# Kernel optimization log

Measured on AMD Instinct MI355X. Metric: run time of the kernel, lower is better.

## Reference

```python
import jax, jax.numpy as jnp
import numpy as np

NEG = -9e15  # matches torch's -9000000000000000.0 masking constant


def setup_inputs() -> dict:
    key = jax.random.key(0)
    kq, kk, kv, ka = jax.random.split(key, 4)
    B, H, N, d = 8, 8, 1024, 128
    queries = jax.random.normal(kq, (B, H, N, d), dtype=jnp.float32)
    keys = jax.random.normal(kk, (B, H, N, d), dtype=jnp.float32)
    values = jax.random.normal(kv, (B, H, N, d), dtype=jnp.float32)
    adj = jax.random.randint(ka, (N, N), 0, 2, dtype=jnp.int32)
    return {"queries": queries, "keys": keys, "values": values, "adj": adj}


def reference(queries, keys, values, adj):
    # scores: [B,H,N,N]; original divides by the constant 8 (not sqrt(dim))
    e = jnp.einsum("bhnd,bhmd->bhnm", queries, keys) / 8.0
    # adjacency mask [N,N] broadcasts over batch and heads
    att = jnp.where(adj > 0, e, jnp.asarray(NEG, e.dtype))
    att = jax.nn.softmax(att, axis=-1)
    # dropout is identity in eval mode
    h = jnp.einsum("bhnm,bhmd->bhnd", att, values)  # [B,H,N,d]
    B, H, N, d = h.shape
    # original uses .view (raw reshape), NOT a permute
    return jnp.reshape(h, (N, B, H, d))
```

## Files before the change

kernel.cpp:

```cpp
#include <hip/hip_runtime.h>
#include <hip/hip_bf16.h>


typedef __bf16 bf16x8 __attribute__((ext_vector_type(8)));
typedef float  f32x4  __attribute__((ext_vector_type(4)));
typedef float  f32x16 __attribute__((ext_vector_type(16)));
typedef unsigned int u32;
typedef u32 u32x4 __attribute__((ext_vector_type(4)));

#define NSEQ 1024
#define DH   128
#define BN   64
#define NKT  16
#define TILE_ELEMS (BN * DH)
#define C1 0.1803368801111244f
#define C2 11.5415603271110070f

__device__ __forceinline__ float f4get(const float4& v, int c) {
    return (c == 0) ? v.x : (c == 1) ? v.y : (c == 2) ? v.z : v.w;
}

__device__ __forceinline__ void gload_lds16(const void* g, void* l) {
    __builtin_amdgcn_global_load_lds(
        (const __attribute__((address_space(1))) u32*)g,
        (__attribute__((address_space(3))) u32*)l, 16, 0, 0);
}

__global__ __launch_bounds__(256)
void prepack_kernel(const float* __restrict__ K, const float* __restrict__ V,
                    __bf16* __restrict__ Kws, __bf16* __restrict__ Vws,
                    u32* __restrict__ adjc, const int* __restrict__ adj)
{
    const int tid = threadIdx.x;
    const int id  = blockIdx.x;

    if (id >= 1024) {
        const int idx  = id - 1024;
        const int rg32 = idx & 31;
        const int kv   = (idx >> 5) * 256 + tid;
        u32 w = 0;
        #pragma unroll
        for (int j = 0; j < 32; ++j)
            w |= (u32)(adj[(size_t)(rg32 * 32 + j) * NSEQ + kv] > 0) << j;
        adjc[(size_t)kv * 32 + rg32] = w;
        return;
    }

    const size_t gbase = (size_t)(id >> 4) * NSEQ * DH + (size_t)(id & 15) * BN * DH;
    __bf16* ko = Kws + (size_t)id * TILE_ELEMS;
    __bf16* vo = Vws + (size_t)id * TILE_ELEMS;

    #pragma unroll
    for (int p = 0; p < 4; ++p) {
        const int r = p * 16 + (tid >> 4);
        const int c = tid & 15;
        const float* src = K + gbase + (size_t)r * DH + c * 8;
        float4 a = *(const float4*)src;
        float4 b = *(const float4*)(src + 4);
        bf16x8 w;
        w[0]=(__bf16)a.x; w[1]=(__bf16)a.y; w[2]=(__bf16)a.z; w[3]=(__bf16)a.w;
        w[4]=(__bf16)b.x; w[5]=(__bf16)b.y; w[6]=(__bf16)b.z; w[7]=(__bf16)b.w;
        const int cs = (c & 8) | ((c ^ (r & 7)) & 7);
        *(bf16x8*)(ko + r * DH + cs * 8) = w;
    }
    {
        const int vkvb = tid >> 5;
        const int vdb  = tid & 31;
        float4 vr[8];
        #pragma unroll
        for (int rr = 0; rr < 8; ++rr)
            vr[rr] = *(const float4*)(V + gbase + (size_t)(vkvb * 8 + rr) * DH + vdb * 4);
        #pragma unroll
        for (int c = 0; c < 4; ++c) {
            const int d = vdb * 4 + c;
            bf16x8 w;
            #pragma unroll
            for (int j = 0; j < 8; ++j) w[j] = (__bf16)f4get(vr[j], c);
            const int cs = vkvb ^ (d & 7);
            *(bf16x8*)(vo + d * BN + cs * 8) = w;
        }
    }
}

__global__ __launch_bounds__(512, 4)
void attn_fast(const float* __restrict__ Q, const __bf16* __restrict__ Kws,
               const __bf16* __restrict__ Vws, const u32* __restrict__ adjc,
               float* __restrict__ out)
{
    __shared__ __attribute__((aligned(16))) __bf16 Kt[2][TILE_ELEMS];
    __shared__ __attribute__((aligned(16))) __bf16 Vt[TILE_ELEMS];
    __shared__ __attribute__((aligned(16))) __bf16 Ps[128 * BN];

    const int tid  = threadIdx.x;
    const int wave = tid >> 6;
    const int lane = tid & 63;
    const int l31  = lane & 31;
    const int hi   = lane >> 5;
    const int l7   = lane & 7;
    const int rowg = wave >> 1;
    const int colg = wave & 1;

    const int id = blockIdx.x;
    const int bh = (id & 7) * 8 + ((id >> 3) & 7);
    const int q0 = (id >> 6) * 128;
    const size_t base  = (size_t)bh * NSEQ * DH;
    const size_t tile0 = (size_t)(bh * NKT) * TILE_ELEMS;

    bf16x8 qf[8];
    {
        const float* qrowp = Q + base + (size_t)(q0 + rowg * 32 + l31) * DH + hi * 8;
        #pragma unroll
        for (int ks = 0; ks < 8; ++ks) {
            const float* src = qrowp + ks * 16;
            float4 a = *(const float4*)src;
            float4 b = *(const float4*)(src + 4);
            bf16x8 w;
            w[0]=(__bf16)a.x; w[1]=(__bf16)a.y; w[2]=(__bf16)a.z; w[3]=(__bf16)a.w;
            w[4]=(__bf16)b.x; w[5]=(__bf16)b.y; w[6]=(__bf16)b.z; w[7]=(__bf16)b.w;
            qf[ks] = w;
            __builtin_amdgcn_sched_barrier(0);
        }
    }

    const size_t ab = (size_t)(colg * 32 + l31) * 32 + (q0 >> 5) + rowg;
    const int kbase = (colg * 32 + l31) * DH * 2;

    f32x16 o0, o1;
    #pragma unroll
    for (int i = 0; i < 16; ++i) { o0[i] = 0.f; o1[i] = 0.f; }
    float rs = 0.f;

    #pragma unroll
    for (int j = 0; j < 2; ++j) {
        const int off = wave * 1024 + j * 512;
        gload_lds16(Kws + tile0 + off + lane * 8, &Kt[0][off]);
    }

    for (int kt = 0; kt < NKT; ++kt) {
        __builtin_amdgcn_sched_barrier(0);
        asm volatile("s_waitcnt vmcnt(0)" ::: "memory");
        __builtin_amdgcn_sched_barrier(0);
        __builtin_amdgcn_s_barrier();
        __builtin_amdgcn_sched_barrier(0);

        const u32 am = adjc[ab + (size_t)kt * 2048];
        __builtin_amdgcn_sched_barrier(0);

        {
            const __bf16* vtile = Vws + tile0 + (size_t)kt * TILE_ELEMS;
            #pragma unroll
            for (int j = 0; j < 2; ++j) {
                const int off = wave * 1024 + j * 512;
                gload_lds16(vtile + off + lane * 8, &Vt[off]);
            }
        }
        __builtin_amdgcn_sched_barrier(0);

        {
            const int ktn = (kt + 1) & (NKT - 1);
            const int st  = (kt == NKT - 1) ? (NKT - 2) : (kt + 1);
            const __bf16* ktile = Kws + tile0 + (size_t)st * TILE_ELEMS;
            __bf16* kdst = &Kt[ktn & 1][0];
            #pragma unroll
            for (int j = 0; j < 2; ++j) {
                const int off = wave * 1024 + j * 512;
                gload_lds16(ktile + off + lane * 8, kdst + off);
            }
        }
        __builtin_amdgcn_sched_barrier(0);

        const __bf16* Kc = &Kt[kt & 1][0];
        f32x16 s;
        #pragma unroll
        for (int i = 0; i < 16; ++i) s[i] = 0.f;
        __builtin_amdgcn_s_setprio(1);
        #pragma unroll
        for (int ks = 0; ks < 8; ++ks) {
            const int c  = ks * 2 + hi;
            const int cs = (c & 8) | ((c ^ l7) & 7);
            bf16x8 bfr = *(const bf16x8*)((const char*)Kc + kbase + cs * 16);
            s = __builtin_amdgcn_mfma_f32_32x32x16_bf16(qf[ks], bfr, s, 0, 0, 0);
        }
        __builtin_amdgcn_s_setprio(0);

        {
            const u32 m2 = am >> (hi * 4);
            const int chunk0 = colg * 4 + (l31 >> 3);
            const int wbase  = (rowg * 32 + 4 * hi) * BN + l7;
            #pragma unroll
            for (int reg = 0; reg < 16; ++reg) {
                const int rlo = (reg & 3) + 8 * (reg >> 2);
                float p = exp2f(__builtin_fmaf(s[reg], C1, -C2));
                p = ((m2 >> rlo) & 1u) ? p : 0.f;
                const int swc = chunk0 ^ ((reg & 3) | (hi << 2));
                Ps[wbase + rlo * BN + swc * 8] = (__bf16)p;
            }
        }

        __builtin_amdgcn_sched_barrier(0);
        asm volatile("s_waitcnt vmcnt(2) lgkmcnt(0)" ::: "memory");
        __builtin_amdgcn_sched_barrier(0);
        __builtin_amdgcn_s_barrier();
        __builtin_amdgcn_sched_barrier(0);

        __builtin_amdgcn_s_setprio(1);
        #pragma unroll
        for (int kstep = 0; kstep < 4; ++kstep) {
            const int chs = (kstep * 2 + hi) ^ l7;
            bf16x8 pa = *(const bf16x8*)(&Ps[(rowg * 32 + l31) * BN + chs * 8]);
            bf16x8 vf0 = *(const bf16x8*)(&Vt[(l31)      * BN + chs * 8 + colg * 64 * BN]);
            o0 = __builtin_amdgcn_mfma_f32_32x32x16_bf16(pa, vf0, o0, 0, 0, 0);
            bf16x8 vf1 = *(const bf16x8*)(&Vt[(32 + l31) * BN + chs * 8 + colg * 64 * BN]);
            o1 = __builtin_amdgcn_mfma_f32_32x32x16_bf16(pa, vf1, o1, 0, 0, 0);
            u32x4 pu = __builtin_bit_cast(u32x4, pa);
            #pragma unroll
            for (int w = 0; w < 4; ++w) {
                const u32 d = pu[w];
                rs += __uint_as_float(d << 16);
                rs += __uint_as_float(d & 0xffff0000u);
            }
        }
        __builtin_amdgcn_s_setprio(0);
    }

    rs += __shfl_xor(rs, 32);
    __syncthreads();
    float* Ls = (float*)&Vt[0];
    if (lane < 32 && colg == 0)
        Ls[rowg * 32 + l31] = rs;
    __syncthreads();
    #pragma unroll
    for (int reg = 0; reg < 16; ++reg) {
        const int row = rowg * 32 + (reg & 3) + 8 * (reg >> 2) + 4 * hi;
        const float linv = 1.0f / fmaxf(Ls[row], 1e-30f);
        float* orow = out + base + (size_t)(q0 + row) * DH + colg * 64 + l31;
        orow[0]  = o0[reg] * linv;
        orow[32] = o1[reg] * linv;
    }
}

#define KS_STRIDE 136
#define VT_STRIDE 64
#define PS_STRIDE 72

__global__ __launch_bounds__(256, 4)
void attn_fallback(const float* __restrict__ Q, const float* __restrict__ K,
                   const float* __restrict__ V, const int* __restrict__ adj,
                   float* __restrict__ out)
{
    __shared__ __attribute__((aligned(16))) __bf16 KsP[BN * KS_STRIDE];
    __shared__ __attribute__((aligned(16))) __bf16 Vts[DH * VT_STRIDE];
    const int tid = threadIdx.x;
    const int wave = tid >> 6, lane = tid & 63, n16 = lane & 15, quad = lane >> 4;
    const int id = blockIdx.x;
    const int bh = (id & 7) * 8 + ((id >> 3) & 7);
    const int q0 = (id >> 6) * 64;
    const size_t base = (size_t)bh * NSEQ * DH;
    const int rp = tid >> 4, kcol = (tid & 15) * 8, db = tid & 31, kvb = tid >> 5;
    bf16x8 qf[4];
    #pragma unroll
    for (int ks = 0; ks < 4; ++ks) {
        const float* src = Q + base + (size_t)(q0 + wave * 16 + n16) * DH + ks * 32 + quad * 8;
        float4 a = *(const float4*)src; float4 b = *(const float4*)(src + 4);
        bf16x8 w;
        w[0]=(__bf16)a.x; w[1]=(__bf16)a.y; w[2]=(__bf16)a.z; w[3]=(__bf16)a.w;
        w[4]=(__bf16)b.x; w[5]=(__bf16)b.y; w[6]=(__bf16)b.z; w[7]=(__bf16)b.w;
        qf[ks] = w;
    }
    f32x4 o[8];
    #pragma unroll
    for (int i = 0; i < 8; ++i) o[i] = (f32x4){0.f, 0.f, 0.f, 0.f};
    float lp[4] = {0.f, 0.f, 0.f, 0.f};
    const int qrow = q0 + wave * 16 + quad * 4;
    for (int kt = 0; kt < NKT; ++kt) {
        const int kv0 = kt * BN;
        __syncthreads();
        #pragma unroll
        for (int it = 0; it < 4; ++it) {
            int row = 16 * it + rp;
            const float* src = K + base + (size_t)(kv0 + row) * DH + kcol;
            float4 a = *(const float4*)src; float4 b = *(const float4*)(src + 4);
            bf16x8 w;
            w[0]=(__bf16)a.x; w[1]=(__bf16)a.y; w[2]=(__bf16)a.z; w[3]=(__bf16)a.w;
            w[4]=(__bf16)b.x; w[5]=(__bf16)b.y; w[6]=(__bf16)b.z; w[7]=(__bf16)b.w;
            *(bf16x8*)(&KsP[row * KS_STRIDE + kcol]) = w;
        }
        {
            float4 vreg[8];
            #pragma unroll
            for (int rr = 0; rr < 8; ++rr)
                vreg[rr] = *(const float4*)(V + base + (size_t)(kv0 + kvb * 8 + rr) * DH + db * 4);
            #pragma unroll
            for (int c = 0; c < 4; ++c) {
                bf16x8 w;
                #pragma unroll
                for (int j = 0; j < 8; ++j) w[j] = (__bf16)f4get(vreg[j], c);
                int d = db * 4 + c, s = (d ^ (d >> 3)) & 7;
                *(bf16x8*)(&Vts[d * VT_STRIDE + ((kvb ^ s) << 3)]) = w;
            }
        }
        __syncthreads();
        int am[4][4];
        #pragma unroll
        for (int i = 0; i < 4; ++i)
            #pragma unroll
            for (int t = 0; t < 4; ++t)
                am[i][t] = adj[(size_t)(qrow + i) * NSEQ + kv0 + t * 16 + n16];
        float sc[4][4];
        #pragma unroll
        for (int t = 0; t < 4; ++t) {
            f32x4 acc = (f32x4){0.f, 0.f, 0.f, 0.f};
            #pragma unroll
            for (int ks = 0; ks < 4; ++ks) {
                bf16x8 bfr = *(const bf16x8*)(&KsP[(t * 16 + n16) * KS_STRIDE + ks * 32 + quad * 8]);
                acc = __builtin_amdgcn_mfma_f32_16x16x32_bf16(qf[ks], bfr, acc, 0, 0, 0);
            }
            #pragma unroll
            for (int i = 0; i < 4; ++i) sc[t][i] = acc[i];
        }
        __syncthreads();
        #pragma unroll
        for (int i = 0; i < 4; ++i) {
            const int prow = wave * 16 + quad * 4 + i;
            float rowsum = 0.f;
            #pragma unroll
            for (int t = 0; t < 4; ++t) {
                float p = exp2f(sc[t][i] * C1 - C2);
                p = (am[i][t] > 0) ? p : 0.f;
                rowsum += p;
                KsP[prow * PS_STRIDE + t * 16 + n16] = (__bf16)p;
            }
            lp[i] += rowsum;
        }
        #pragma unroll
        for (int ks = 0; ks < 2; ++ks) {
            bf16x8 pf = *(const bf16x8*)(&KsP[(wave * 16 + n16) * PS_STRIDE + ks * 32 + quad * 8]);
            #pragma unroll
            for (int nt = 0; nt < 8; ++nt) {
                int d = nt * 16 + n16, s = (d ^ (d >> 3)) & 7, kvbr = ks * 4 + quad;
                bf16x8 vf = *(const bf16x8*)(&Vts[d * VT_STRIDE + ((kvbr ^ s) << 3)]);
                o[nt] = __builtin_amdgcn_mfma_f32_16x16x32_bf16(pf, vf, o[nt], 0, 0, 0);
            }
        }
    }
    float linv[4];
    #pragma unroll
    for (int i = 0; i < 4; ++i) {
        float ls = lp[i];
        ls += __shfl_xor(ls, 1); ls += __shfl_xor(ls, 2);
        ls += __shfl_xor(ls, 4); ls += __shfl_xor(ls, 8);
        linv[i] = 1.0f / fmaxf(ls, 1e-30f);
    }
    #pragma unroll
    for (int nt = 0; nt < 8; ++nt)
        #pragma unroll
        for (int i = 0; i < 4; ++i)
            out[base + (size_t)(qrow + i) * DH + nt * 16 + n16] = o[nt][i] * linv[i];
}

extern "C" void kernel_launch(void* const* d_in, const int* in_sizes, int n_in,
                              void* d_out, int out_size, void* d_ws, size_t ws_size,
                              hipStream_t stream) {
    const float* Q   = (const float*)d_in[0];
    const float* K   = (const float*)d_in[1];
    const float* V   = (const float*)d_in[2];
    const int*   adj = (const int*)d_in[3];
    float* out = (float*)d_out;
    const size_t needKV  = (size_t)2 * 64 * NKT * TILE_ELEMS * sizeof(__bf16);
    const size_t needAdj = (size_t)NSEQ * 32 * sizeof(u32);
    if (ws_size >= needKV + needAdj) {
        __bf16* Kws = (__bf16*)d_ws;
        __bf16* Vws = Kws + (size_t)64 * NKT * TILE_ELEMS;
        u32* adjc = (u32*)(Vws + (size_t)64 * NKT * TILE_ELEMS);
        prepack_kernel<<<1152, 256, 0, stream>>>(K, V, Kws, Vws, adjc, adj);
        attn_fast<<<512, 512, 0, stream>>>(Q, Kws, Vws, adjc, out);
    } else {
        attn_fallback<<<1024, 256, 0, stream>>>(Q, K, V, adj, out);
    }
}
```

Before: 210.9 us.

## Rewrite fast attention with 128-wide KV tiles and 1024-thread blocks

Replaces the 64-wide KV tiling with 128-wide tiles and a 16-wave block where each wave owns a 32x32 output block. Q now lives in padded LDS instead of registers, and K/V tiles are staged through registers into padded LDS rather than via direct global-to-LDS loads with XOR swizzles. The prepack kernel emits unswizzled 128x128 tiles. The aim is to halve loop iterations and barriers per tile and to cut per-wave accumulator registers, at the cost of more LDS traffic for Q and an extra barrier per iteration.

Result: slower. 415.9 us (+97.2%).

```diff
diff --git a/kernel.cpp b/kernel.cpp
--- a/kernel.cpp
+++ b/kernel.cpp
@@ -10,32 +10,35 @@
 
 #define NSEQ 1024
 #define DH   128
-#define BN   64
-#define NKT  16
-#define TILE_ELEMS (BN * DH)
 #define C1 0.1803368801111244f
 #define C2 11.5415603271110070f
+#define LD2 130
+#define NT2 8
+#define TILE2 (128 * 128)
 
 __device__ __forceinline__ float f4get(const float4& v, int c) {
     return (c == 0) ? v.x : (c == 1) ? v.y : (c == 2) ? v.z : v.w;
 }
 
-__device__ __forceinline__ void gload_lds16(const void* g, void* l) {
-    __builtin_amdgcn_global_load_lds(
-        (const __attribute__((address_space(1))) u32*)g,
-        (__attribute__((address_space(3))) u32*)l, 16, 0, 0);
+__device__ __forceinline__ bf16x8 cvt8(const float* src) {
+    float4 a = *(const float4*)src;
+    float4 b = *(const float4*)(src + 4);
+    bf16x8 w;
+    w[0]=(__bf16)a.x; w[1]=(__bf16)a.y; w[2]=(__bf16)a.z; w[3]=(__bf16)a.w;
+    w[4]=(__bf16)b.x; w[5]=(__bf16)b.y; w[6]=(__bf16)b.z; w[7]=(__bf16)b.w;
+    return w;
 }
 
 __global__ __launch_bounds__(256)
-void prepack_kernel(const float* __restrict__ K, const float* __restrict__ V,
-                    __bf16* __restrict__ Kws, __bf16* __restrict__ Vws,
-                    u32* __restrict__ adjc, const int* __restrict__ adj)
+void prepack2(const float* __restrict__ K, const float* __restrict__ V,
+              __bf16* __restrict__ Kws, __bf16* __restrict__ Vws,
+              u32* __restrict__ adjc, const int* __restrict__ adj)
 {
     const int tid = threadIdx.x;
     const int id  = blockIdx.x;
 
-    if (id >= 1024) {
-        const int idx  = id - 1024;
+    if (id >= 512) {
+        const int idx  = id - 512;
         const int rg32 = idx & 31;
         const int kv   = (idx >> 5) * 256 + tid;
         u32 w = 0;
@@ -46,172 +49,150 @@
         return;
     }
 
-    const size_t gbase = (size_t)(id >> 4) * NSEQ * DH + (size_t)(id & 15) * BN * DH;
-    __bf16* ko = Kws + (size_t)id * TILE_ELEMS;
-    __bf16* vo = Vws + (size_t)id * TILE_ELEMS;
-
-    #pragma unroll
-    for (int p = 0; p < 4; ++p) {
+    const size_t gbase = (size_t)(id >> 3) * NSEQ * DH + (size_t)(id & 7) * 128 * DH;
+    __bf16* ko = Kws + (size_t)id * TILE2;
+    __bf16* vo = Vws + (size_t)id * TILE2;
+
+    #pragma unroll
+    for (int p = 0; p < 8; ++p) {
         const int r = p * 16 + (tid >> 4);
         const int c = tid & 15;
-        const float* src = K + gbase + (size_t)r * DH + c * 8;
-        float4 a = *(const float4*)src;
-        float4 b = *(const float4*)(src + 4);
-        bf16x8 w;
-        w[0]=(__bf16)a.x; w[1]=(__bf16)a.y; w[2]=(__bf16)a.z; w[3]=(__bf16)a.w;
-        w[4]=(__bf16)b.x; w[5]=(__bf16)b.y; w[6]=(__bf16)b.z; w[7]=(__bf16)b.w;
-        const int cs = (c & 8) | ((c ^ (r & 7)) & 7);
-        *(bf16x8*)(ko + r * DH + cs * 8) = w;
+        *(bf16x8*)(ko + r * 128 + c * 8) = cvt8(K + gbase + (size_t)r * DH + c * 8);
     }
     {
-        const int vkvb = tid >> 5;
-        const int vdb  = tid & 31;
-        float4 vr[8];
-        #pragma unroll
-        for (int rr = 0; rr < 8; ++rr)
-            vr[rr] = *(const float4*)(V + gbase + (size_t)(vkvb * 8 + rr) * DH + vdb * 4);
-        #pragma unroll
-        for (int c = 0; c < 4; ++c) {
-            const int d = vdb * 4 + c;
-            bf16x8 w;
-            #pragma unroll
-            for (int j = 0; j < 8; ++j) w[j] = (__bf16)f4get(vr[j], c);
-            const int cs = vkvb ^ (d & 7);
-            *(bf16x8*)(vo + d * BN + cs * 8) = w;
-        }
-    }
-}
-
-__global__ __launch_bounds__(512, 4)
-void attn_fast(const float* __restrict__ Q, const __bf16* __restrict__ Kws,
-               const __bf16* __restrict__ Vws, const u32* __restrict__ adjc,
-               float* __restrict__ out)
+        const int vdb = tid & 31;
+        const int vkb = tid >> 5;
+        #pragma unroll
+        for (int pass = 0; pass < 2; ++pass) {
+            float4 vr[8];
+            #pragma unroll
+            for (int j = 0; j < 8; ++j)
+                vr[j] = *(const float4*)(V + gbase
+                         + (size_t)(vkb * 16 + pass * 8 + j) * DH + vdb * 4);
+            #pragma unroll
+            for (int c = 0; c < 4; ++c) {
+                const int d = vdb * 4 + c;
+                bf16x8 w;
+                #pragma unroll
+                for (int j = 0; j < 8; ++j) w[j] = (__bf16)f4get(vr[j], c);
+                *(bf16x8*)(vo + d * 128 + vkb * 16 + pass * 8) = w;
+            }
+        }
+    }
+}
+
+__global__ __launch_bounds__(1024, 4)
+void attn_big(const float* __restrict__ Q, const __bf16* __restrict__ Kws,
+              const __bf16* __restrict__ Vws, const u32* __restrict__ adjc,
+              float* __restrict__ out)
 {
-    __shared__ __attribute__((aligned(16))) __bf16 Kt[2][TILE_ELEMS];
-    __shared__ __attribute__((aligned(16))) __bf16 Vt[TILE_ELEMS];
-    __shared__ __attribute__((aligned(16))) __bf16 Ps[128 * BN];
+    __shared__ __attribute__((aligned(16))) __bf16 Qs[128 * LD2];
+    __shared__ __attribute__((aligned(16))) __bf16 Kt[128 * LD2];
+    __shared__ __attribute__((aligned(16))) __bf16 Vt[128 * LD2];
+    __shared__ __attribute__((aligned(16))) __bf16 Ps[128 * LD2];
 
     const int tid  = threadIdx.x;
     const int wave = tid >> 6;
     const int lane = tid & 63;
     const int l31  = lane & 31;
     const int hi   = lane >> 5;
-    const int l7   = lane & 7;
-    const int rowg = wave >> 1;
-    const int colg = wave & 1;
+    const int rowg = wave >> 2;
+    const int cg   = wave & 3;
 
     const int id = blockIdx.x;
     const int bh = (id & 7) * 8 + ((id >> 3) & 7);
     const int q0 = (id >> 6) * 128;
-    const size_t base  = (size_t)bh * NSEQ * DH;
-    const size_t tile0 = (size_t)(bh * NKT) * TILE_ELEMS;
-
-    bf16x8 qf[8];
+    const size_t base = (size_t)bh * NSEQ * DH;
+
+    const int sr = tid >> 4;
+    const int sc = (tid & 15) * 8;
+    const __bf16* kg = Kws + (size_t)(bh * NT2) * TILE2 + sr * 128 + sc;
+    const __bf16* vg = Vws + (size_t)(bh * NT2) * TILE2 + sr * 128 + sc;
+    __bf16* kd0 = &Kt[sr * LD2 + sc];
+    __bf16* kd1 = &Kt[(64 + sr) * LD2 + sc];
+    __bf16* vd0 = &Vt[sr * LD2 + sc];
+    __bf16* vd1 = &Vt[(64 + sr) * LD2 + sc];
+
+    const __bf16* qr = &Qs[(rowg * 32 + l31) * LD2 + hi * 8];
+    const __bf16* kr = &Kt[(cg * 32 + l31) * LD2 + hi * 8];
+    const __bf16* pr = &Ps[(rowg * 32 + l31) * LD2 + hi * 8];
+    const __bf16* vp = &Vt[(cg * 32 + l31) * LD2 + hi * 8];
+    __bf16* pw = &Ps[(rowg * 32 + 4 * hi) * LD2 + cg * 32 + l31];
+    const u32* ap = adjc + (size_t)(cg * 32 + l31) * 32 + (q0 >> 5) + rowg;
+
+    f32x16 o;
+    #pragma unroll
+    for (int i = 0; i < 16; ++i) o[i] = 0.f;
+    float rs = 0.f;
+
     {
-        const float* qrowp = Q + base + (size_t)(q0 + rowg * 32 + l31) * DH + hi * 8;
-        #pragma unroll
-        for (int ks = 0; ks < 8; ++ks) {
-            const float* src = qrowp + ks * 16;
-            float4 a = *(const float4*)src;
-            float4 b = *(const float4*)(src + 4);
-            bf16x8 w;
-            w[0]=(__bf16)a.x; w[1]=(__bf16)a.y; w[2]=(__bf16)a.z; w[3]=(__bf16)a.w;
-            w[4]=(__bf16)b.x; w[5]=(__bf16)b.y; w[6]=(__bf16)b.z; w[7]=(__bf16)b.w;
-            qf[ks] = w;
-            __builtin_amdgcn_sched_barrier(0);
-        }
-    }
-
-    const size_t ab = (size_t)(colg * 32 + l31) * 32 + (q0 >> 5) + rowg;
-    const int kbase = (colg * 32 + l31) * DH * 2;
-
-    f32x16 o0, o1;
-    #pragma unroll
-    for (int i = 0; i < 16; ++i) { o0[i] = 0.f; o1[i] = 0.f; }
-    float rs = 0.f;
-
-    #pragma unroll
-    for (int j = 0; j < 2; ++j) {
-        const int off = wave * 1024 + j * 512;
-        gload_lds16(Kws + tile0 + off + lane * 8, &Kt[0][off]);
-    }
-
-    for (int kt = 0; kt < NKT; ++kt) {
-        __builtin_amdgcn_sched_barrier(0);
-        asm volatile("s_waitcnt vmcnt(0)" ::: "memory");
-        __builtin_amdgcn_sched_barrier(0);
+        const float* qsrc = Q + base + (size_t)(q0 + (tid >> 3)) * DH + (tid & 7) * 16;
+        __bf16* qdst = &Qs[(tid >> 3) * LD2 + (tid & 7) * 16];
+        *(bf16x8*)qdst       = cvt8(qsrc);
+        *(bf16x8*)(qdst + 8) = cvt8(qsrc + 8);
+        bf16x8 ka = *(const bf16x8*)(kg);
+        bf16x8 kb = *(const bf16x8*)(kg + 8192);
+        bf16x8 va = *(const bf16x8*)(vg);
+        bf16x8 vb = *(const bf16x8*)(vg + 8192);
+        *(bf16x8*)kd0 = ka;  *(bf16x8*)kd1 = kb;
+        *(bf16x8*)vd0 = va;  *(bf16x8*)vd1 = vb;
+    }
+
+    for (int kt = 0; kt < NT2; ++kt) {
+        __builtin_amdgcn_sched_barrier(0);
+        asm volatile("s_waitcnt lgkmcnt(0)" ::: "memory");
         __builtin_amdgcn_s_barrier();
         __builtin_amdgcn_sched_barrier(0);
 
-        const u32 am = adjc[ab + (size_t)kt * 2048];
-        __builtin_amdgcn_sched_barrier(0);
-
-        {
-            const __bf16* vtile = Vws + tile0 + (size_t)kt * TILE_ELEMS;
-            #pragma unroll
-            for (int j = 0; j < 2; ++j) {
-                const int off = wave * 1024 + j * 512;
-                gload_lds16(vtile + off + lane * 8, &Vt[off]);
-            }
-        }
-        __builtin_amdgcn_sched_barrier(0);
-
-        {
-            const int ktn = (kt + 1) & (NKT - 1);
-            const int st  = (kt == NKT - 1) ? (NKT - 2) : (kt + 1);
-            const __bf16* ktile = Kws + tile0 + (size_t)st * TILE_ELEMS;
-            __bf16* kdst = &Kt[ktn & 1][0];
-            #pragma unroll
-            for (int j = 0; j < 2; ++j) {
-                const int off = wave * 1024 + j * 512;
-                gload_lds16(ktile + off + lane * 8, kdst + off);
-            }
-        }
-        __builtin_amdgcn_sched_barrier(0);
-
-        const __bf16* Kc = &Kt[kt & 1][0];
+        const u32 am = ap[kt * 4096];
+
+        const int st = (kt < NT2 - 1) ? (kt + 1) : (NT2 - 1);
+        const __bf16* kgs = kg + (size_t)st * TILE2;
+        const __bf16* vgs = vg + (size_t)st * TILE2;
+        bf16x8 ka = *(const bf16x8*)(kgs);
+        bf16x8 kb = *(const bf16x8*)(kgs + 8192);
+        bf16x8 va = *(const bf16x8*)(vgs);
+        bf16x8 vb = *(const bf16x8*)(vgs + 8192);
+        __builtin_amdgcn_sched_barrier(0);
+
         f32x16 s;
         #pragma unroll
         for (int i = 0; i < 16; ++i) s[i] = 0.f;
         __builtin_amdgcn_s_setprio(1);
         #pragma unroll
         for (int ks = 0; ks < 8; ++ks) {
-            const int c  = ks * 2 + hi;
-            const int cs = (c & 8) | ((c ^ l7) & 7);
-            bf16x8 bfr = *(const bf16x8*)((const char*)Kc + kbase + cs * 16);
-            s = __builtin_amdgcn_mfma_f32_32x32x16_bf16(qf[ks], bfr, s, 0, 0, 0);
+            bf16x8 qa = *(const bf16x8*)(qr + ks * 16);
+            bf16x8 kf = *(const bf16x8*)(kr + ks * 16);
+            s = __builtin_amdgcn_mfma_f32_32x32x16_bf16(qa, kf, s, 0, 0, 0);
         }
         __builtin_amdgcn_s_setprio(0);
 
         {
             const u32 m2 = am >> (hi * 4);
-            const int chunk0 = colg * 4 + (l31 >> 3);
-            const int wbase  = (rowg * 32 + 4 * hi) * BN + l7;
             #pragma unroll
             for (int reg = 0; reg < 16; ++reg) {
                 const int rlo = (reg & 3) + 8 * (reg >> 2);
                 float p = exp2f(__builtin_fmaf(s[reg], C1, -C2));
                 p = ((m2 >> rlo) & 1u) ? p : 0.f;
-                const int swc = chunk0 ^ ((reg & 3) | (hi << 2));
-                Ps[wbase + rlo * BN + swc * 8] = (__bf16)p;
-            }
-        }
-
-        __builtin_amdgcn_sched_barrier(0);
-        asm volatile("s_waitcnt vmcnt(2) lgkmcnt(0)" ::: "memory");
-        __builtin_amdgcn_sched_barrier(0);
+                pw[rlo * LD2] = (__bf16)p;
+            }
+        }
+
+        __builtin_amdgcn_sched_barrier(0);
+        asm volatile("s_waitcnt lgkmcnt(0)" ::: "memory");
         __builtin_amdgcn_s_barrier();
         __builtin_amdgcn_sched_barrier(0);
 
+        *(bf16x8*)kd0 = ka;
+        *(bf16x8*)kd1 = kb;
+        __builtin_amdgcn_sched_barrier(0);
+
         __builtin_amdgcn_s_setprio(1);
         #pragma unroll
-        for (int kstep = 0; kstep < 4; ++kstep) {
-            const int chs = (kstep * 2 + hi) ^ l7;
-            bf16x8 pa = *(const bf16x8*)(&Ps[(rowg * 32 + l31) * BN + chs * 8]);
-            bf16x8 vf0 = *(const bf16x8*)(&Vt[(l31)      * BN + chs * 8 + colg * 64 * BN]);
-            o0 = __builtin_amdgcn_mfma_f32_32x32x16_bf16(pa, vf0, o0, 0, 0, 0);
-            bf16x8 vf1 = *(const bf16x8*)(&Vt[(32 + l31) * BN + chs * 8 + colg * 64 * BN]);
-            o1 = __builtin_amdgcn_mfma_f32_32x32x16_bf16(pa, vf1, o1, 0, 0, 0);
+        for (int kstep = 0; kstep < 8; ++kstep) {
+            bf16x8 pa = *(const bf16x8*)(pr + kstep * 16);
+            bf16x8 vf = *(const bf16x8*)(vp + kstep * 16);
+            o = __builtin_amdgcn_mfma_f32_32x32x16_bf16(pa, vf, o, 0, 0, 0);
             u32x4 pu = __builtin_bit_cast(u32x4, pa);
             #pragma unroll
             for (int w = 0; w < 4; ++w) {
@@ -221,24 +202,30 @@
             }
         }
         __builtin_amdgcn_s_setprio(0);
+
+        __builtin_amdgcn_sched_barrier(0);
+        __builtin_amdgcn_s_barrier();
+        __builtin_amdgcn_sched_barrier(0);
+        *(bf16x8*)vd0 = va;
+        *(bf16x8*)vd1 = vb;
     }
 
     rs += __shfl_xor(rs, 32);
     __syncthreads();
-    float* Ls = (float*)&Vt[0];
-    if (lane < 32 && colg == 0)
+    float* Ls = (float*)&Ps[0];
+    if (cg == 0 && lane < 32)
         Ls[rowg * 32 + l31] = rs;
     __syncthreads();
     #pragma unroll
     for (int reg = 0; reg < 16; ++reg) {
         const int row = rowg * 32 + (reg & 3) + 8 * (reg >> 2) + 4 * hi;
         const float linv = 1.0f / fmaxf(Ls[row], 1e-30f);
-        float* orow = out + base + (size_t)(q0 + row) * DH + colg * 64 + l31;
-        orow[0]  = o0[reg] * linv;
-        orow[32] = o1[reg] * linv;
-    }
-}
-
+        out[base + (size_t)(q0 + row) * DH + cg * 32 + l31] = o[reg] * linv;
+    }
+}
+
+#define BN 64
+#define NKT 16
 #define KS_STRIDE 136
 #define VT_STRIDE 64
 #define PS_STRIDE 72
@@ -259,14 +246,8 @@
     const int rp = tid >> 4, kcol = (tid & 15) * 8, db = tid & 31, kvb = tid >> 5;
     bf16x8 qf[4];
     #pragma unroll
-    for (int ks = 0; ks < 4; ++ks) {
-        const float* src = Q + base + (size_t)(q0 + wave * 16 + n16) * DH + ks * 32 + quad * 8;
-        float4 a = *(const float4*)src; float4 b = *(const float4*)(src + 4);
-        bf16x8 w;
-        w[0]=(__bf16)a.x; w[1]=(__bf16)a.y; w[2]=(__bf16)a.z; w[3]=(__bf16)a.w;
-        w[4]=(__bf16)b.x; w[5]=(__bf16)b.y; w[6]=(__bf16)b.z; w[7]=(__bf16)b.w;
-        qf[ks] = w;
-    }
+    for (int ks = 0; ks < 4; ++ks)
+        qf[ks] = cvt8(Q + base + (size_t)(q0 + wave * 16 + n16) * DH + ks * 32 + quad * 8);
     f32x4 o[8];
     #pragma unroll
     for (int i = 0; i < 8; ++i) o[i] = (f32x4){0.f, 0.f, 0.f, 0.f};
@@ -278,12 +259,8 @@
         #pragma unroll
         for (int it = 0; it < 4; ++it) {
             int row = 16 * it + rp;
-            const float* src = K + base + (size_t)(kv0 + row) * DH + kcol;
-            float4 a = *(const float4*)src; float4 b = *(const float4*)(src + 4);
-            bf16x8 w;
-            w[0]=(__bf16)a.x; w[1]=(__bf16)a.y; w[2]=(__bf16)a.z; w[3]=(__bf16)a.w;
-            w[4]=(__bf16)b.x; w[5]=(__bf16)b.y; w[6]=(__bf16)b.z; w[7]=(__bf16)b.w;
-            *(bf16x8*)(&KsP[row * KS_STRIDE + kcol]) = w;
+            *(bf16x8*)(&KsP[row * KS_STRIDE + kcol]) =
+                cvt8(K + base + (size_t)(kv0 + row) * DH + kcol);
         }
         {
             float4 vreg[8];
@@ -366,14 +343,14 @@
     const float* V   = (const float*)d_in[2];
     const int*   adj = (const int*)d_in[3];
     float* out = (float*)d_out;
-    const size_t needKV  = (size_t)2 * 64 * NKT * TILE_ELEMS * sizeof(__bf16);
-    const size_t needAdj = (size_t)NSEQ * 32 * sizeof(u32);
-    if (ws_size >= needKV + needAdj) {
+    const size_t nKV  = (size_t)2 * 64 * NT2 * TILE2 * sizeof(__bf16);
+    const size_t nAdj = (size_t)NSEQ * 32 * sizeof(u32);
+    if (ws_size >= nKV + nAdj) {
         __bf16* Kws = (__bf16*)d_ws;
-        __bf16* Vws = Kws + (size_t)64 * NKT * TILE_ELEMS;
-        u32* adjc = (u32*)(Vws + (size_t)64 * NKT * TILE_ELEMS);
-        prepack_kernel<<<1152, 256, 0, stream>>>(K, V, Kws, Vws, adjc, adj);
-        attn_fast<<<512, 512, 0, stream>>>(Q, Kws, Vws, adjc, out);
+        __bf16* Vws = Kws + (size_t)64 * NT2 * TILE2;
+        u32* adjc = (u32*)(Vws + (size_t)64 * NT2 * TILE2);
+        prepack2<<<640, 256, 0, stream>>>(K, V, Kws, Vws, adjc, adj);
+        attn_big<<<512, 1024, 0, stream>>>(Q, Kws, Vws, adjc, out);
     } else {
         attn_fallback<<<1024, 256, 0, stream>>>(Q, K, V, adj, out);
     }
```
